# Performance work log

Measured on AMD Instinct MI355X. Metric: run time of the kernel, lower is better.

Reference implementation:

```python
import jax, jax.numpy as jnp
import numpy as np

N_NODES = 100000
N_EDGES = 1600000
HIDDEN = 64
FILTERS = 64
GAUSS = 5
SHORT = 5
N_CONV = 2
Z_DIM = 2 * FILTERS + SHORT  # CGConv concat [x_i, x_j, e]


def setup_inputs() -> dict:
    key = jax.random.key(0)
    ks = jax.random.split(key, 12)
    h = jax.random.normal(ks[0], (N_NODES, HIDDEN), dtype=jnp.float32)
    edge_index = jax.random.randint(ks[1], (2, N_EDGES), 0, N_NODES, dtype=jnp.int64)
    edge_weight = jax.random.uniform(ks[2], (N_EDGES,), dtype=jnp.float32)
    edge_attr = jax.random.uniform(ks[3], (N_EDGES, GAUSS), dtype=jnp.float32)
    s = 1.0 / np.sqrt(HIDDEN)
    lin0_w = jax.random.uniform(ks[4], (HIDDEN, FILTERS), jnp.float32, -s, s)
    lin0_b = jax.random.uniform(ks[5], (FILTERS,), jnp.float32, -s, s)
    s2 = 1.0 / np.sqrt(GAUSS)
    short_w = jax.random.uniform(ks[6], (GAUSS, SHORT), jnp.float32, -s2, s2)
    short_b = jax.random.uniform(ks[7], (SHORT,), jnp.float32, -s2, s2)
    s3 = 1.0 / np.sqrt(Z_DIM)
    conv_f_w = jax.random.uniform(ks[8], (N_CONV, Z_DIM, FILTERS), jnp.float32, -s3, s3)
    conv_f_b = jax.random.uniform(ks[9], (N_CONV, FILTERS), jnp.float32, -s3, s3)
    conv_s_w = jax.random.uniform(ks[10], (N_CONV, Z_DIM, FILTERS), jnp.float32, -s3, s3)
    conv_s_b = jax.random.uniform(ks[11], (N_CONV, FILTERS), jnp.float32, -s3, s3)
    return {
        'h': h, 'edge_index': edge_index, 'edge_weight': edge_weight,
        'edge_attr': edge_attr, 'data': 0,
        'lin0_w': lin0_w, 'lin0_b': lin0_b,
        'short_w': short_w, 'short_b': short_b,
        'conv_f_w': conv_f_w, 'conv_f_b': conv_f_b,
        'conv_s_w': conv_s_w, 'conv_s_b': conv_s_b,
    }


def _cgconv(x, src, dst, e, wf, bf, ws, bs):
    # z = [x_i, x_j, e]; split the matmul to avoid materializing z[E, 2F+5]
    x_i = x[dst]  # target node features [E, F]
    x_j = x[src]  # source node features [E, F]
    F_ = x.shape[1]
    zf = x_i @ wf[:F_] + x_j @ wf[F_:2 * F_] + e @ wf[2 * F_:] + bf
    zs = x_i @ ws[:F_] + x_j @ ws[F_:2 * F_] + e @ ws[2 * F_:] + bs
    msg = jax.nn.sigmoid(zf) * jax.nn.softplus(zs)  # gated messages [E, F]
    agg = jax.ops.segment_sum(msg, dst, num_segments=x.shape[0])
    return x + agg  # residual, aggr='add', batch_norm=False


def reference(h, edge_index, edge_weight, edge_attr, data,
              lin0_w, lin0_b, short_w, short_b,
              conv_f_w, conv_f_b, conv_s_w, conv_s_b):
    out = jax.nn.relu(h @ lin0_w + lin0_b)          # [N, F]
    e = jax.nn.relu(edge_attr @ short_w + short_b)  # [E, 5]
    src, dst = edge_index[0], edge_index[1]
    for i in range(N_CONV):
        out = jax.nn.relu(_cgconv(out, src, dst, e,
                                  conv_f_w[i], conv_f_b[i],
                                  conv_s_w[i], conv_s_b[i]))
    return out
```

## Files before the change

kernel.cpp:

```cpp
#include <hip/hip_runtime.h>

#define NN 100000
#define NE 1600000
#define NSB 391

#define LOG2E 1.4426950408889634f
#define LN2 0.6931471805599453f

typedef short short4v __attribute__((ext_vector_type(4)));
typedef short short8v __attribute__((ext_vector_type(8)));
typedef float f32x2 __attribute__((ext_vector_type(2)));
typedef float f32x4 __attribute__((ext_vector_type(4)));
typedef unsigned u32x4 __attribute__((ext_vector_type(4)));

static __device__ __forceinline__ unsigned f2bf(float x) {
    unsigned b = __float_as_uint(x);
    return (b + 0x7FFFu + ((b >> 16) & 1u)) >> 16;
}
static __device__ __forceinline__ float bflo(unsigned u) { return __uint_as_float(u << 16); }
static __device__ __forceinline__ float bfhi(unsigned u) { return __uint_as_float(u & 0xFFFF0000u); }
static __device__ __forceinline__ int imin(int a, int b) { return a < b ? a : b; }
static __device__ __forceinline__ short8v mk8(short4v a, short4v b) {
    short8v r;
    r[0] = a[0]; r[1] = a[1]; r[2] = a[2]; r[3] = a[3];
    r[4] = b[0]; r[5] = b[1]; r[6] = b[2]; r[7] = b[3];
    return r;
}

static __device__ __forceinline__ int swz(int row, int colblk) {
    return row * 64 + ((colblk ^ (row & 7)) << 3);
}

static __device__ __forceinline__ void frag_reads(const short* xl, int row, int g,
                                                  short8v& a0, short8v& a1) {
    const int sub = (g & 1) * 4;
    const int cb = g >> 1;
    const short4v p0 = *(const short4v*)&xl[swz(row, cb + 0) + sub];
    const short4v p1 = *(const short4v*)&xl[swz(row, cb + 2) + sub];
    const short4v p2 = *(const short4v*)&xl[swz(row, cb + 4) + sub];
    const short4v p3 = *(const short4v*)&xl[swz(row, cb + 6) + sub];
    a0 = mk8(p0, p1);
    a1 = mk8(p2, p3);
}

static __device__ __forceinline__ float edge_acc(uint4 m, unsigned ps, f32x2 pd2,
                                                 const f32x2* __restrict__ w2, float acc) {
    f32x2 z = __builtin_amdgcn_cvt_pk_f32_fp8((int)ps, false);
    z += pd2;
    const float e50 = bflo(m.y), e51 = bfhi(m.y);
    const float e52 = bflo(m.z), e53 = bfhi(m.z);
    const float e54 = bflo(m.w);
    z += e50 * w2[0];
    z += e51 * w2[1];
    z += e52 * w2[2];
    z += e53 * w2[3];
    z += e54 * w2[4];
    const float sig = __builtin_amdgcn_rcpf(1.f + __builtin_amdgcn_exp2f(z.x));
    const float gg = __builtin_amdgcn_logf(1.f + __builtin_amdgcn_exp2f(z.y));
    return fmaf(sig, gg, acc);
}

__global__ __launch_bounds__(256) void k_wpack(const float* __restrict__ cfw,
                                               const float* __restrict__ csw,
                                               const float* __restrict__ l0w,
                                               unsigned short* __restrict__ Bp) {
    const int qq = blockIdx.x * 256 + threadIdx.x;
    const float* src;
    float scale;
    int roff, ct, kh, l;
    if (qq < 4096) {
        const int layer = qq >> 11;
        const int q = qq & 2047;
        const int m = q >> 9;
        const int rem = q & 511;
        ct = rem >> 7;
        kh = (rem >> 6) & 1;
        l = rem & 63;
        scale = (m & 1) ? LOG2E : -LOG2E;
        src = ((m & 1) ? csw : cfw) + (size_t)layer * 133 * 64;
        roff = (m >> 1) ? 64 : 0;
    } else {
        const int p = qq - 4096;
        ct = p >> 7;
        kh = (p >> 6) & 1;
        l = p & 63;
        scale = 1.f;
        src = l0w;
        roff = 0;
    }
    const int n = ct * 16 + (l & 15);
#pragma unroll
    for (int j = 0; j < 8; j++) {
        const int k = kh * 32 + ((j < 4) ? (4 * (l >> 4) + j) : (16 + 4 * (l >> 4) + j - 4));
        Bp[(size_t)qq * 8 + j] = (unsigned short)f2bf(scale * src[(size_t)(roff + k) * 64 + n]);
    }
}

__global__ __launch_bounds__(256) void k_lin0m_hist(const float* __restrict__ h,
                                                    const unsigned short* __restrict__ Bp0,
                                                    const float* __restrict__ b,
                                                    unsigned short* __restrict__ xb,
                                                    const int* __restrict__ ei,
                                                    int* __restrict__ cnt,
                                                    int* __restrict__ rank) {
    __shared__ __align__(16) short xl[32 * 64];
    const int r7 = blockIdx.x % 7;
    const int q7 = blockIdx.x / 7;
    if (r7 < 2) {
        const int base = (q7 * 2 + r7) * 1280 + threadIdx.x;
        int r[5];
#pragma unroll
        for (int j = 0; j < 5; j++) r[j] = atomicAdd(&cnt[ei[NE + base + j * 256]], 1);
#pragma unroll
        for (int j = 0; j < 5; j++) rank[base + j * 256] = r[j];
        return;
    }
    const int rowbase = (q7 * 5 + (r7 - 2)) * 32;
    {
        const float4* hs = (const float4*)(h + (size_t)rowbase * 64);
#pragma unroll
        for (int it = 0; it < 2; it++) {
            const int i = threadIdx.x + it * 256;
            const float4 v = hs[i];
            short4v sv;
            sv[0] = (short)f2bf(v.x);
            sv[1] = (short)f2bf(v.y);
            sv[2] = (short)f2bf(v.z);
            sv[3] = (short)f2bf(v.w);
            const int row = i >> 4;
            *(short4v*)&xl[swz(row, (i >> 1) & 7) + (i & 1) * 4] = sv;
        }
    }
    __syncthreads();
    const int ct = threadIdx.x >> 6;
    const int l = threadIdx.x & 63;
    const int lm = l & 15;
    const int g = l >> 4;
    short8v A[2][2];
#pragma unroll
    for (int rt = 0; rt < 2; rt++) frag_reads(xl, rt * 16 + lm, g, A[rt][0], A[rt][1]);
    const short* bp = (const short*)Bp0;
    const short8v B0 = *(const short8v*)&bp[((ct * 2 + 0) * 64 + l) * 8];
    const short8v B1 = *(const short8v*)&bp[((ct * 2 + 1) * 64 + l) * 8];
    const int col = ct * 16 + lm;
    const float bc = b[col];
#pragma unroll
    for (int rt = 0; rt < 2; rt++) {
        f32x4 a = {0.f, 0.f, 0.f, 0.f};
        a = __builtin_amdgcn_mfma_f32_16x16x32_bf16(A[rt][0], B0, a, 0, 0, 0);
        a = __builtin_amdgcn_mfma_f32_16x16x32_bf16(A[rt][1], B1, a, 0, 0, 0);
#pragma unroll
        for (int reg = 0; reg < 4; reg++) {
            const int rowg = rowbase + rt * 16 + g * 4 + reg;
            xb[(size_t)rowg * 64 + col] = (unsigned short)f2bf(fmaxf(a[reg] + bc, 0.f));
        }
    }
}

__global__ __launch_bounds__(256) void k_scan1(const int* __restrict__ cnt,
                                               int* __restrict__ offs, int* __restrict__ bsum) {
    __shared__ int sm[256];
    const int t = threadIdx.x;
    const int i = blockIdx.x * 256 + t;
    const int v = (i < NN) ? cnt[i] : 0;
    sm[t] = v;
    __syncthreads();
    for (int off = 1; off < 256; off <<= 1) {
        const int x = (t >= off) ? sm[t - off] : 0;
        __syncthreads();
        sm[t] += x;
        __syncthreads();
    }
    if (i < NN) offs[i] = sm[t] - v;
    if (t == 255) bsum[blockIdx.x] = sm[255];
}

__global__ __launch_bounds__(512) void k_scan2(int* __restrict__ bsum) {
    __shared__ int sm[512];
    const int t = threadIdx.x;
    const int v = (t < NSB) ? bsum[t] : 0;
    sm[t] = v;
    __syncthreads();
    for (int off = 1; off < 512; off <<= 1) {
        const int x = (t >= off) ? sm[t - off] : 0;
        __syncthreads();
        sm[t] += x;
        __syncthreads();
    }
    if (t < NSB) bsum[t] = sm[t] - v;
}

__global__ __launch_bounds__(256) void k_scan3(int* __restrict__ offs,
                                               const int* __restrict__ bsum) {
    const int i = blockIdx.x * 256 + threadIdx.x;
    if (i < NN) offs[i] += bsum[blockIdx.x];
    if (i == 0) offs[NN] = NE;
}

__global__ __launch_bounds__(256) void k_scat_proj(const int* __restrict__ ei,
                                                   const float* __restrict__ eattr,
                                                   const float* __restrict__ sw,
                                                   const float* __restrict__ sb,
                                                   const int* __restrict__ rank,
                                                   const int* __restrict__ offs,
                                                   unsigned* __restrict__ meta,
                                                   const unsigned short* __restrict__ xb,
                                                   const unsigned short* __restrict__ Bp,
                                                   const float* __restrict__ bfv,
                                                   const float* __restrict__ bsv,
                                                   unsigned* __restrict__ Pd,
                                                   unsigned short* __restrict__ Ps8) {
    __shared__ __align__(16) short xl[32 * 64];
    const int r7 = blockIdx.x % 7;
    const int q7 = blockIdx.x / 7;
    if (r7 < 2) {
        __shared__ float swl[25], sbl[5];
        if (threadIdx.x < 25) swl[threadIdx.x] = sw[threadIdx.x];
        if (threadIdx.x >= 32 && threadIdx.x < 37) sbl[threadIdx.x - 32] = sb[threadIdx.x - 32];
        __syncthreads();
        const int base = (q7 * 2 + r7) * 1280 + threadIdx.x;
        int s[5], d[5], r[5];
        float ea[5][5];
#pragma unroll
        for (int j = 0; j < 5; j++) {
            const int e = base + j * 256;
            s[j] = ei[e];
            d[j] = ei[NE + e];
            r[j] = rank[e];
#pragma unroll
            for (int k = 0; k < 5; k++) ea[j][k] = eattr[(size_t)e * 5 + k];
        }
        int pos[5];
#pragma unroll
        for (int j = 0; j < 5; j++) pos[j] = offs[d[j]] + r[j];
#pragma unroll
        for (int j = 0; j < 5; j++) {
            unsigned u5[5];
#pragma unroll
            for (int k = 0; k < 5; k++) {
                float a = sbl[k];
#pragma unroll
                for (int q = 0; q < 5; q++) a += ea[j][q] * swl[q * 5 + k];
                u5[k] = f2bf(fmaxf(a, 0.f));
            }
            u32x4 m;
            m[0] = (unsigned)s[j];
            m[1] = u5[0] | (u5[1] << 16);
            m[2] = u5[2] | (u5[3] << 16);
            m[3] = u5[4];
            __builtin_nontemporal_store(m, (u32x4*)&meta[(size_t)pos[j] * 4]);
        }
        return;
    }
    const int rowbase = (q7 * 5 + (r7 - 2)) * 32;
    {
        const u32x4* xsrc = (const u32x4*)(xb + (size_t)rowbase * 64);
        const int i = threadIdx.x;
        const u32x4 v = __builtin_nontemporal_load(&xsrc[i]);
        *(u32x4*)&xl[swz(i >> 3, i & 7)] = v;
    }
    __syncthreads();
    const int ct = threadIdx.x >> 6;
    const int l = threadIdx.x & 63;
    const int lm = l & 15;
    const int g = l >> 4;
    short8v A[2][2];
#pragma unroll
    for (int rt = 0; rt < 2; rt++) frag_reads(xl, rt * 16 + lm, g, A[rt][0], A[rt][1]);
    const short* bp = (const short*)Bp;
    f32x4 acc[4][2];
#pragma unroll
    for (int m = 0; m < 4; m++) {
        const short8v B0 = *(const short8v*)&bp[(((m * 4 + ct) * 2 + 0) * 64 + l) * 8];
        const short8v B1 = *(const short8v*)&bp[(((m * 4 + ct) * 2 + 1) * 64 + l) * 8];
#pragma unroll
        for (int rt = 0; rt < 2; rt++) {
            f32x4 a = {0.f, 0.f, 0.f, 0.f};
            a = __builtin_amdgcn_mfma_f32_16x16x32_bf16(A[rt][0], B0, a, 0, 0, 0);
            a = __builtin_amdgcn_mfma_f32_16x16x32_bf16(A[rt][1], B1, a, 0, 0, 0);
            acc[m][rt] = a;
        }
    }
    const int col = ct * 16 + lm;
    const float bfb = -LOG2E * bfv[col];
    const float bsb = LOG2E * bsv[col];
#pragma unroll
    for (int rt = 0; rt < 2; rt++) {
#pragma unroll
        for (int reg = 0; reg < 4; reg++) {
            const int rowg = rowbase + rt * 16 + g * 4 + reg;
            Pd[(size_t)rowg * 64 + col] =
                f2bf(acc[0][rt][reg] + bfb) | (f2bf(acc[1][rt][reg] + bsb) << 16);
            Ps8[(size_t)rowg * 64 + col] = (unsigned short)__builtin_amdgcn_cvt_pk_fp8_f32(
                acc[2][rt][reg], acc[3][rt][reg], 0, false);
        }
    }
}

__global__ __launch_bounds__(256) void k_projm(const unsigned short* __restrict__ xb,
                                               const unsigned short* __restrict__ Bp,
                                               const float* __restrict__ bfv,
                                               const float* __restrict__ bsv,
                                               unsigned* __restrict__ Pd,
                                               unsigned short* __restrict__ Ps8) {
    __shared__ __align__(16) short xl[32 * 64];
    const int rowbase = blockIdx.x * 32;
    {
        const u32x4* xsrc = (const u32x4*)(xb + (size_t)rowbase * 64);
        const int i = threadIdx.x;
        const u32x4 v = __builtin_nontemporal_load(&xsrc[i]);
        *(u32x4*)&xl[swz(i >> 3, i & 7)] = v;
    }
    __syncthreads();
    const int ct = threadIdx.x >> 6;
    const int l = threadIdx.x & 63;
    const int lm = l & 15;
    const int g = l >> 4;
    short8v A[2][2];
#pragma unroll
    for (int rt = 0; rt < 2; rt++) frag_reads(xl, rt * 16 + lm, g, A[rt][0], A[rt][1]);
    const short* bp = (const short*)Bp;
    f32x4 acc[4][2];
#pragma unroll
    for (int m = 0; m < 4; m++) {
        const short8v B0 = *(const short8v*)&bp[(((m * 4 + ct) * 2 + 0) * 64 + l) * 8];
        const short8v B1 = *(const short8v*)&bp[(((m * 4 + ct) * 2 + 1) * 64 + l) * 8];
#pragma unroll
        for (int rt = 0; rt < 2; rt++) {
            f32x4 a = {0.f, 0.f, 0.f, 0.f};
            a = __builtin_amdgcn_mfma_f32_16x16x32_bf16(A[rt][0], B0, a, 0, 0, 0);
            a = __builtin_amdgcn_mfma_f32_16x16x32_bf16(A[rt][1], B1, a, 0, 0, 0);
            acc[m][rt] = a;
        }
    }
    const int col = ct * 16 + lm;
    const float bfb = -LOG2E * bfv[col];
    const float bsb = LOG2E * bsv[col];
#pragma unroll
    for (int rt = 0; rt < 2; rt++) {
#pragma unroll
        for (int reg = 0; reg < 4; reg++) {
            const int rowg = rowbase + rt * 16 + g * 4 + reg;
            Pd[(size_t)rowg * 64 + col] =
                f2bf(acc[0][rt][reg] + bfb) | (f2bf(acc[1][rt][reg] + bsb) << 16);
            Ps8[(size_t)rowg * 64 + col] = (unsigned short)__builtin_amdgcn_cvt_pk_fp8_f32(
                acc[2][rt][reg], acc[3][rt][reg], 0, false);
        }
    }
}

__global__ __launch_bounds__(64) void k_seg(const int* __restrict__ offs,
                                            const uint4* __restrict__ meta,
                                            const unsigned* __restrict__ Pd,
                                            const unsigned short* __restrict__ Ps8,
                                            const float* __restrict__ wfE,
                                            const float* __restrict__ wsE,
                                            const unsigned short* __restrict__ xbin,
                                            float* __restrict__ outf,
                                            unsigned short* __restrict__ xbout) {
    const int n = blockIdx.x;
    const int lane = threadIdx.x;
    const int start = __builtin_amdgcn_readfirstlane(offs[n]);
    const int end = __builtin_amdgcn_readfirstlane(offs[n + 1]);
    const unsigned pd = __builtin_nontemporal_load(&Pd[(size_t)n * 64 + lane]);
    f32x2 pd2;
    pd2.x = bflo(pd);
    pd2.y = bfhi(pd);
    f32x2 w2[5];
#pragma unroll
    for (int k = 0; k < 5; k++) {
        f32x2 p;
        p.x = -LOG2E * wfE[k * 64 + lane];
        p.y = LOG2E * wsE[k * 64 + lane];
        w2[k] = p;
    }
    const float xv = bflo((unsigned)xbin[(size_t)n * 64 + lane]);
    float acc0 = 0.f, acc1 = 0.f;
    const int cnt = end - start;
    if (cnt > 0) {
        const int last = end - 1;
        const int nbF = (cnt + 3) >> 2;
        uint4 M0[4], M1[4];
        unsigned PS0[4];
#pragma unroll
        for (int j = 0; j < 4; j++) M0[j] = meta[imin(start + j, last)];
#pragma unroll
        for (int j = 0; j < 4; j++) M1[j] = meta[imin(start + 4 + j, last)];
#pragma unroll
        for (int j = 0; j < 4; j++) PS0[j] = Ps8[(size_t)M0[j].x * 64 + lane];
        for (int b = 0; b < nbF - 1; b++) {
            const int base2 = __builtin_amdgcn_readfirstlane(start + (b + 2) * 4);
            uint4 M2[4];
            unsigned PS1[4];
#pragma unroll
            for (int j = 0; j < 4; j++) M2[j] = meta[imin(base2 + j, last)];
#pragma unroll
            for (int j = 0; j < 4; j++) PS1[j] = Ps8[(size_t)M1[j].x * 64 + lane];
            acc0 = edge_acc(M0[0], PS0[0], pd2, w2, acc0);
            acc1 = edge_acc(M0[1], PS0[1], pd2, w2, acc1);
            acc0 = edge_acc(M0[2], PS0[2], pd2, w2, acc0);
            acc1 = edge_acc(M0[3], PS0[3], pd2, w2, acc1);
#pragma unroll
            for (int j = 0; j < 4; j++) {
                M0[j] = M1[j];
                M1[j] = M2[j];
                PS0[j] = PS1[j];
            }
        }
        const int lb = start + (nbF - 1) * 4;
        if (lb + 0 < end) acc0 = edge_acc(M0[0], PS0[0], pd2, w2, acc0);
        if (lb + 1 < end) acc1 = edge_acc(M0[1], PS0[1], pd2, w2, acc1);
        if (lb + 2 < end) acc0 = edge_acc(M0[2], PS0[2], pd2, w2, acc0);
        if (lb + 3 < end) acc1 = edge_acc(M0[3], PS0[3], pd2, w2, acc1);
    }
    const float res = fmaxf(fmaf(acc0 + acc1, LN2, xv), 0.f);
    if (outf) {
        __builtin_nontemporal_store(res, &outf[(size_t)n * 64 + lane]);
    } else {
        xbout[(size_t)n * 64 + lane] = (unsigned short)f2bf(res);
    }
}

extern "C" void kernel_launch(void* const* d_in, const int* in_sizes, int n_in,
                              void* d_out, int out_size, void* d_ws, size_t ws_size,
                              hipStream_t stream) {
    const float* h = (const float*)d_in[0];
    const int* ei = (const int*)d_in[1];
    const float* eattr = (const float*)d_in[3];
    const float* lin0_w = (const float*)d_in[5];
    const float* lin0_b = (const float*)d_in[6];
    const float* short_w = (const float*)d_in[7];
    const float* short_b = (const float*)d_in[8];
    const float* conv_f_w = (const float*)d_in[9];
    const float* conv_f_b = (const float*)d_in[10];
    const float* conv_s_w = (const float*)d_in[11];
    const float* conv_s_b = (const float*)d_in[12];

    char* ws = (char*)d_ws;
    uint4* meta = (uint4*)ws;
    unsigned* Pd = (unsigned*)(ws + (size_t)NE * 16);
    unsigned short* Ps8 = (unsigned short*)(Pd + (size_t)NN * 64);
    unsigned short* XB = Ps8 + (size_t)NN * 64;
    unsigned short* Bp = XB + (size_t)NN * 64;
    int* cnt = (int*)(Bp + 36864);
    int* offs = cnt + NN;
    int* bsum = offs + NN + 1;
    int* rank = bsum + NSB;

    hipMemsetAsync(cnt, 0, (size_t)NN * 4, stream);
    k_wpack<<<18, 256, 0, stream>>>(conv_f_w, conv_s_w, lin0_w, Bp);
    k_lin0m_hist<<<4375, 256, 0, stream>>>(h, Bp + 32768, lin0_b, XB, ei, cnt, rank);
    k_scan1<<<NSB, 256, 0, stream>>>(cnt, offs, bsum);
    k_scan2<<<1, 512, 0, stream>>>(bsum);
    k_scan3<<<NSB, 256, 0, stream>>>(offs, bsum);
    k_scat_proj<<<4375, 256, 0, stream>>>(ei, eattr, short_w, short_b, rank, offs,
                                          (unsigned*)meta, XB, Bp, conv_f_b, conv_s_b,
                                          Pd, Ps8);
    k_seg<<<NN, 64, 0, stream>>>(offs, meta, Pd, Ps8,
                                 conv_f_w + 128 * 64, conv_s_w + 128 * 64,
                                 XB, nullptr, XB);
    k_projm<<<NN / 32, 256, 0, stream>>>(XB, Bp + 16384, conv_f_b + 64, conv_s_b + 64, Pd, Ps8);
    k_seg<<<NN, 64, 0, stream>>>(offs, meta, Pd, Ps8,
                                 conv_f_w + 133 * 64 + 128 * 64,
                                 conv_s_w + 133 * 64 + 128 * 64,
                                 XB, (float*)d_out, nullptr);
}
```

Baseline: 309.1 us.

## Pack edge metadata into 8 bytes with fp8 features and deepen prefetch

Per-edge metadata shrinks from 16 bytes (source index plus five bf16 short features) to 8 bytes: the source index sits in the low 24 bits and the five projected edge features are stored as fp8, with the fifth in the top byte of the index word. The segment kernel unpacks them with hardware fp8-to-f32 conversions and adds another stage to the software pipeline, so metadata is prefetched three blocks ahead and Ps8 gathers two blocks ahead. This cuts the metadata traffic written once and read in both conv layers, and gives more time to hide gather latency. In exchange, edge features lose precision in fp8, node indices are limited to 24 bits, and more registers are live per thread.

```diff
diff --git a/kernel.cpp b/kernel.cpp
--- a/kernel.cpp
+++ b/kernel.cpp
@@ -11,6 +11,7 @@
 typedef short short8v __attribute__((ext_vector_type(8)));
 typedef float f32x2 __attribute__((ext_vector_type(2)));
 typedef float f32x4 __attribute__((ext_vector_type(4)));
+typedef unsigned u32x2 __attribute__((ext_vector_type(2)));
 typedef unsigned u32x4 __attribute__((ext_vector_type(4)));
 
 static __device__ __forceinline__ unsigned f2bf(float x) {
@@ -18,7 +19,6 @@
     return (b + 0x7FFFu + ((b >> 16) & 1u)) >> 16;
 }
 static __device__ __forceinline__ float bflo(unsigned u) { return __uint_as_float(u << 16); }
-static __device__ __forceinline__ float bfhi(unsigned u) { return __uint_as_float(u & 0xFFFF0000u); }
 static __device__ __forceinline__ int imin(int a, int b) { return a < b ? a : b; }
 static __device__ __forceinline__ short8v mk8(short4v a, short4v b) {
     short8v r;
@@ -43,18 +43,18 @@
     a1 = mk8(p2, p3);
 }
 
-static __device__ __forceinline__ float edge_acc(uint4 m, unsigned ps, f32x2 pd2,
+static __device__ __forceinline__ float edge_acc(u32x2 m, unsigned ps, f32x2 pd2,
                                                  const f32x2* __restrict__ w2, float acc) {
     f32x2 z = __builtin_amdgcn_cvt_pk_f32_fp8((int)ps, false);
     z += pd2;
-    const float e50 = bflo(m.y), e51 = bfhi(m.y);
-    const float e52 = bflo(m.z), e53 = bfhi(m.z);
-    const float e54 = bflo(m.w);
-    z += e50 * w2[0];
-    z += e51 * w2[1];
-    z += e52 * w2[2];
-    z += e53 * w2[3];
-    z += e54 * w2[4];
+    const f32x2 e01 = __builtin_amdgcn_cvt_pk_f32_fp8((int)m.y, false);
+    const f32x2 e23 = __builtin_amdgcn_cvt_pk_f32_fp8((int)m.y, true);
+    const f32x2 e4x = __builtin_amdgcn_cvt_pk_f32_fp8((int)(m.x >> 24), false);
+    z += e01.x * w2[0];
+    z += e01.y * w2[1];
+    z += e23.x * w2[2];
+    z += e23.y * w2[3];
+    z += e4x.x * w2[4];
     const float sig = __builtin_amdgcn_rcpf(1.f + __builtin_amdgcn_exp2f(z.x));
     const float gg = __builtin_amdgcn_logf(1.f + __builtin_amdgcn_exp2f(z.y));
     return fmaf(sig, gg, acc);
@@ -203,7 +203,7 @@
                                                    const float* __restrict__ sb,
                                                    const int* __restrict__ rank,
                                                    const int* __restrict__ offs,
-                                                   unsigned* __restrict__ meta,
+                                                   u32x2* __restrict__ meta,
                                                    const unsigned short* __restrict__ xb,
                                                    const unsigned short* __restrict__ Bp,
                                                    const float* __restrict__ bfv,
@@ -235,20 +235,22 @@
         for (int j = 0; j < 5; j++) pos[j] = offs[d[j]] + r[j];
 #pragma unroll
         for (int j = 0; j < 5; j++) {
-            unsigned u5[5];
+            float e5[5];
 #pragma unroll
             for (int k = 0; k < 5; k++) {
                 float a = sbl[k];
 #pragma unroll
                 for (int q = 0; q < 5; q++) a += ea[j][q] * swl[q * 5 + k];
-                u5[k] = f2bf(fmaxf(a, 0.f));
+                e5[k] = fmaxf(a, 0.f);
             }
-            u32x4 m;
-            m[0] = (unsigned)s[j];
-            m[1] = u5[0] | (u5[1] << 16);
-            m[2] = u5[2] | (u5[3] << 16);
-            m[3] = u5[4];
-            __builtin_nontemporal_store(m, (u32x4*)&meta[(size_t)pos[j] * 4]);
+            unsigned hi = (unsigned)__builtin_amdgcn_cvt_pk_fp8_f32(e5[0], e5[1], 0, false);
+            hi = (unsigned)__builtin_amdgcn_cvt_pk_fp8_f32(e5[2], e5[3], (int)hi, true);
+            const unsigned b4 =
+                (unsigned)__builtin_amdgcn_cvt_pk_fp8_f32(e5[4], 0.f, 0, false) & 0xFFu;
+            u32x2 m;
+            m.x = (unsigned)s[j] | (b4 << 24);
+            m.y = hi;
+            meta[pos[j]] = m;
         }
         return;
     }
@@ -350,7 +352,7 @@
 }
 
 __global__ __launch_bounds__(64) void k_seg(const int* __restrict__ offs,
-                                            const uint4* __restrict__ meta,
+                                            const u32x2* __restrict__ meta,
                                             const unsigned* __restrict__ Pd,
                                             const unsigned short* __restrict__ Ps8,
                                             const float* __restrict__ wfE,
@@ -365,7 +367,7 @@
     const unsigned pd = __builtin_nontemporal_load(&Pd[(size_t)n * 64 + lane]);
     f32x2 pd2;
     pd2.x = bflo(pd);
-    pd2.y = bfhi(pd);
+    pd2.y = __uint_as_float(pd & 0xFFFF0000u);
     f32x2 w2[5];
 #pragma unroll
     for (int k = 0; k < 5; k++) {
@@ -380,22 +382,26 @@
     if (cnt > 0) {
         const int last = end - 1;
         const int nbF = (cnt + 3) >> 2;
-        uint4 M0[4], M1[4];
-        unsigned PS0[4];
+        u32x2 M0[4], M1[4], M2[4];
+        unsigned PS0[4], PS1[4];
 #pragma unroll
         for (int j = 0; j < 4; j++) M0[j] = meta[imin(start + j, last)];
 #pragma unroll
         for (int j = 0; j < 4; j++) M1[j] = meta[imin(start + 4 + j, last)];
 #pragma unroll
-        for (int j = 0; j < 4; j++) PS0[j] = Ps8[(size_t)M0[j].x * 64 + lane];
+        for (int j = 0; j < 4; j++) M2[j] = meta[imin(start + 8 + j, last)];
+#pragma unroll
+        for (int j = 0; j < 4; j++) PS0[j] = Ps8[(size_t)(M0[j].x & 0xFFFFFFu) * 64 + lane];
+#pragma unroll
+        for (int j = 0; j < 4; j++) PS1[j] = Ps8[(size_t)(M1[j].x & 0xFFFFFFu) * 64 + lane];
         for (int b = 0; b < nbF - 1; b++) {
-            const int base2 = __builtin_amdgcn_readfirstlane(start + (b + 2) * 4);
-            uint4 M2[4];
-            unsigned PS1[4];
-#pragma unroll
-            for (int j = 0; j < 4; j++) M2[j] = meta[imin(base2 + j, last)];
-#pragma unroll
-            for (int j = 0; j < 4; j++) PS1[j] = Ps8[(size_t)M1[j].x * 64 + lane];
+            const int base3 = __builtin_amdgcn_readfirstlane(start + (b + 3) * 4);
+            u32x2 M3[4];
+            unsigned PS2[4];
+#pragma unroll
+            for (int j = 0; j < 4; j++) M3[j] = meta[imin(base3 + j, last)];
+#pragma unroll
+            for (int j = 0; j < 4; j++) PS2[j] = Ps8[(size_t)(M2[j].x & 0xFFFFFFu) * 64 + lane];
             acc0 = edge_acc(M0[0], PS0[0], pd2, w2, acc0);
             acc1 = edge_acc(M0[1], PS0[1], pd2, w2, acc1);
             acc0 = edge_acc(M0[2], PS0[2], pd2, w2, acc0);
@@ -404,7 +410,9 @@
             for (int j = 0; j < 4; j++) {
                 M0[j] = M1[j];
                 M1[j] = M2[j];
+                M2[j] = M3[j];
                 PS0[j] = PS1[j];
+                PS1[j] = PS2[j];
             }
         }
         const int lb = start + (nbF - 1) * 4;
@@ -437,8 +445,8 @@
     const float* conv_s_b = (const float*)d_in[12];
 
     char* ws = (char*)d_ws;
-    uint4* meta = (uint4*)ws;
-    unsigned* Pd = (unsigned*)(ws + (size_t)NE * 16);
+    u32x2* meta = (u32x2*)ws;
+    unsigned* Pd = (unsigned*)(ws + (size_t)NE * 8);
     unsigned short* Ps8 = (unsigned short*)(Pd + (size_t)NN * 64);
     unsigned short* XB = Ps8 + (size_t)NN * 64;
     unsigned short* Bp = XB + (size_t)NN * 64;
@@ -454,8 +462,7 @@
     k_scan2<<<1, 512, 0, stream>>>(bsum);
     k_scan3<<<NSB, 256, 0, stream>>>(offs, bsum);
     k_scat_proj<<<4375, 256, 0, stream>>>(ei, eattr, short_w, short_b, rank, offs,
-                                          (unsigned*)meta, XB, Bp, conv_f_b, conv_s_b,
-                                          Pd, Ps8);
+                                          meta, XB, Bp, conv_f_b, conv_s_b, Pd, Ps8);
     k_seg<<<NN, 64, 0, stream>>>(offs, meta, Pd, Ps8,
                                  conv_f_w + 128 * 64, conv_s_w + 128 * 64,
                                  XB, nullptr, XB);
```

Result: faster. 298.7 us (-3.4%).
